# Kernel tuning notes

Measured on AMD Instinct MI355X. Metric: run time of the kernel, lower is better.

Reference implementation:

```python
import jax, jax.numpy as jnp
import numpy as np

# Hyperparameters from init_kwargs
SMOOTHNESS = 0.5
RADIUS_RATIO = 0.1  # computed in original code but never used in the mask math
IMG_SIZE = 512
BATCH = 32


def _smooth_mask(h, w, smoothness):
    """Vectorized replacement of the original per-pixel double loop.

    mask[i,j] = smoothness                       if |i-ch|^2 + |j-cw|^2 <= 1
              = max(1, dist_norm / smoothness)   otherwise
    where dist_norm = sqrt((|i-ch|/(h/2))^2 + (|j-cw|/(w/2))^2).
    Returns [h, w] float32 (broadcasts over the channel dim).
    """
    dh = jnp.abs(jnp.arange(h, dtype=jnp.float32) - (h // 2))[:, None]  # [h,1]
    dw = jnp.abs(jnp.arange(w, dtype=jnp.float32) - (w // 2))[None, :]  # [1,w]
    center = dh * dh + dw * dw <= 1.0
    dist = jnp.sqrt((dh / (h / 2)) ** 2 + (dw / (w / 2)) ** 2)
    outer = jnp.maximum(jnp.float32(1.0), dist / smoothness)
    return jnp.where(center, jnp.float32(smoothness), outer)


def setup_inputs() -> dict:
    key = jax.random.key(0)
    kx, = jax.random.split(key, 1)
    x = jax.random.normal(kx, (BATCH, 3, IMG_SIZE, IMG_SIZE), dtype=jnp.float32)
    param = jnp.ones((3, IMG_SIZE, IMG_SIZE), dtype=jnp.float32)  # nn.Parameter init
    return {"x": x, "param": param}


def reference(x, param):
    # x: [B, C, H, W] real -> complex spectrum, centered
    f = jnp.fft.fftshift(jnp.fft.fft2(x), axes=(-2, -1))
    h, w = x.shape[-2], x.shape[-1]
    mask = _smooth_mask(h, w, SMOOTHNESS)          # [H, W]
    filt = f * mask * param                        # broadcast [3,H,W] over batch
    out = jnp.fft.ifft2(jnp.fft.ifftshift(filt, axes=(-2, -1))).real
    return out
```

## Files before the change

### kernel.cpp

```cpp
#include <hip/hip_runtime.h>
#include <math.h>

#define N 512
#define CS 514
#define S8 0.70710678118654752440f

__device__ __forceinline__ float2 cadd(float2 a, float2 b){ return make_float2(a.x+b.x, a.y+b.y); }
__device__ __forceinline__ float2 csub(float2 a, float2 b){ return make_float2(a.x-b.x, a.y-b.y); }
__device__ __forceinline__ float2 cmul(float2 a, float2 b){
    return make_float2(fmaf(a.x,b.x,-(a.y*b.y)), fmaf(a.x,b.y, a.y*b.x));
}
template<int INV> __device__ __forceinline__ float2 rot90(float2 a){
    return INV ? make_float2(-a.y, a.x) : make_float2(a.y, -a.x);
}
template<int INV> __device__ __forceinline__ float2 rotW1(float2 a){
    return INV ? make_float2(S8*(a.x-a.y), S8*(a.x+a.y))
               : make_float2(S8*(a.x+a.y), S8*(a.y-a.x));
}
template<int INV> __device__ __forceinline__ float2 rotW3(float2 a){
    return INV ? make_float2(-S8*(a.x+a.y), S8*(a.x-a.y))
               : make_float2(S8*(a.y-a.x), -S8*(a.x+a.y));
}

template<int INV>
__device__ __forceinline__ void fft8(float2 v[8]) {
    float2 t0 = cadd(v[0],v[4]), t4 = csub(v[0],v[4]);
    float2 t1 = cadd(v[1],v[5]), t5 = rotW1<INV>(csub(v[1],v[5]));
    float2 t2 = cadd(v[2],v[6]), t6 = rot90<INV>(csub(v[2],v[6]));
    float2 t3 = cadd(v[3],v[7]), t7 = rotW3<INV>(csub(v[3],v[7]));
    float2 u0 = cadd(t0,t2), u2 = csub(t0,t2);
    float2 u1 = cadd(t1,t3), u3 = rot90<INV>(csub(t1,t3));
    float2 u4 = cadd(t4,t6), u6 = csub(t4,t6);
    float2 u5 = cadd(t5,t7), u7 = rot90<INV>(csub(t5,t7));
    v[0]=cadd(u0,u1); v[4]=csub(u0,u1);
    v[2]=cadd(u2,u3); v[6]=csub(u2,u3);
    v[1]=cadd(u4,u5); v[5]=csub(u4,u5);
    v[3]=cadd(u6,u7); v[7]=csub(u6,u7);
}

__device__ __forceinline__ void apply_pow(float2 v[8], float2 w1) {
    float2 w2 = cmul(w1,w1);
    float2 w3 = cmul(w2,w1);
    float2 w4 = cmul(w2,w2);
    v[1]=cmul(v[1],w1); v[2]=cmul(v[2],w2); v[3]=cmul(v[3],w3); v[4]=cmul(v[4],w4);
    v[5]=cmul(v[5],cmul(w4,w1));
    v[6]=cmul(v[6],cmul(w4,w2));
    v[7]=cmul(v[7],cmul(w4,w3));
}

__device__ __forceinline__ void fill_tw(float2* tw, int k) {
    float ang = -6.28318530717958647692f * (float)k / (float)N;
    float s, c; sincosf(ang, &s, &c);
    tw[k] = make_float2(c, s);
}

__device__ __forceinline__ void fft512_fwd(float2 v[8], int l, float2* sc, const float2* tw) {
    int hi = l >> 3, lo = l & 7;
    fft8<0>(v);
    apply_pow(v, tw[l]);
#pragma unroll
    for (int q = 0; q < 8; ++q) sc[q*64 + ((hi ^ q) << 3) + lo] = v[q];
#pragma unroll
    for (int b = 0; b < 8; ++b) v[b] = sc[hi*64 + ((b ^ hi) << 3) + lo];
    fft8<0>(v);
    apply_pow(v, tw[lo << 3]);
#pragma unroll
    for (int q2 = 0; q2 < 8; ++q2) sc[q2*64 + ((hi ^ q2) << 3) + (lo ^ hi)] = v[q2];
#pragma unroll
    for (int c = 0; c < 8; ++c) v[c] = sc[hi*64 + ((lo ^ hi) << 3) + (c ^ lo)];
    fft8<0>(v);
}

__device__ __forceinline__ void fft512_inv(float2 v[8], int l, float2* sc, const float2* tw) {
    int hi = l >> 3, lo = l & 7;
    fft8<1>(v);
#pragma unroll
    for (int c = 0; c < 8; ++c) sc[hi*64 + ((lo ^ hi) << 3) + (c ^ lo)] = v[c];
#pragma unroll
    for (int q2 = 0; q2 < 8; ++q2) v[q2] = sc[q2*64 + ((hi ^ q2) << 3) + (lo ^ hi)];
    {
        float2 w = tw[lo << 3];
        apply_pow(v, make_float2(w.x, -w.y));
    }
    fft8<1>(v);
#pragma unroll
    for (int b = 0; b < 8; ++b) sc[hi*64 + ((b ^ hi) << 3) + lo] = v[b];
#pragma unroll
    for (int q = 0; q < 8; ++q) v[q] = sc[q*64 + ((hi ^ q) << 3) + lo];
    {
        float2 w = tw[l];
        apply_pow(v, make_float2(w.x, -w.y));
    }
    fft8<1>(v);
}

__global__ __launch_bounds__(512) void k_filt(const float* __restrict__ param,
                                              float* __restrict__ filt) {
    int c = blockIdx.x >> 9;
    int vv = blockIdx.x & 511;
    int u = threadIdx.x;
    int dh = (u < 256) ? u : (512 - u);
    int dw = (vv < 256) ? vv : (512 - vv);
    int d2 = dh * dh + dw * dw;
    float m = (d2 <= 1) ? 0.5f : fmaxf(1.0f, sqrtf((float)d2) * (2.0f / 256.0f));
    int su  = (u + 256) & 511,  sv  = (vv + 256) & 511;
    int su2 = (256 - u) & 511,  sv2 = (256 - vv) & 511;
    float p  = param[((size_t)c * N + su)  * N + sv];
    float p2 = param[((size_t)c * N + su2) * N + sv2];
    const float invN2 = 1.0f / ((float)N * (float)N);
    filt[(((size_t)c << 9) + vv) * N + u] = m * 0.5f * (p + p2) * invN2;
}

__global__ __launch_bounds__(256) void k_row_fwd(const float* __restrict__ x,
                                                 float2* __restrict__ ws, int pairBase) {
    __shared__ float2 scr[4 * 512];
    __shared__ float2 tw[512];
    int t = threadIdx.x;
    int l = t & 63, wv = t >> 6;
    fill_tw(tw, t); fill_tw(tw, t + 256);
    __syncthreads();
    int pr = blockIdx.x >> 7;
    int row = ((blockIdx.x & 127) << 2) + wv;
    int pair = pairBase + pr;
    const float* xa = x + ((size_t)pair * N + row) * N;
    const float* xb = x + ((size_t)(pair + 48) * N + row) * N;
    float2 v[8];
#pragma unroll
    for (int a = 0; a < 8; ++a) v[a] = make_float2(xa[a * 64 + l], xb[a * 64 + l]);
    fft512_fwd(v, l, scr + wv * 512, tw);
    float2* o = ws + ((size_t)pr * N + row) * N;
#pragma unroll
    for (int r = 0; r < 8; ++r) o[r * 64 + l] = v[r];
}

__global__ __launch_bounds__(512) void k_col(float2* __restrict__ ws,
                                             const float* __restrict__ filt, int pairBase) {
    __shared__ float2 tile[8 * CS];
    __shared__ float2 tw[512];
    int t = threadIdx.x;
    int l = t & 63, wv = t >> 6;
    fill_tw(tw, t);
    int pr = blockIdx.x >> 6;
    int colBase = (blockIdx.x & 63) << 3;
    float2* wsImg = ws + (size_t)pr * (size_t)(N * N);

#pragma unroll
    for (int k = 0; k < 8; ++k) {
        int lin = (k << 9) + t;
        int r = lin >> 3, c = lin & 7;
        tile[c * CS + r] = wsImg[(size_t)r * N + colBase + c];
    }
    __syncthreads();

    float2* sc = tile + wv * CS;
    float2 v[8];
#pragma unroll
    for (int a = 0; a < 8; ++a) v[a] = sc[a * 64 + l];

    fft512_fwd(v, l, sc, tw);

    int ch = (pairBase + pr) % 3;
    int col = colBase + wv;
    const float* fcol = filt + (((size_t)ch << 9) + col) * N;
#pragma unroll
    for (int r = 0; r < 8; ++r) {
        float f = fcol[r * 64 + l];
        v[r].x *= f; v[r].y *= f;
    }

    fft512_inv(v, l, sc, tw);

#pragma unroll
    for (int a = 0; a < 8; ++a) sc[a * 64 + l] = v[a];
    __syncthreads();

#pragma unroll
    for (int k = 0; k < 8; ++k) {
        int lin = (k << 9) + t;
        int r = lin >> 3, c = lin & 7;
        wsImg[(size_t)r * N + colBase + c] = tile[c * CS + r];
    }
}

__global__ __launch_bounds__(256) void k_row_inv(const float2* __restrict__ ws,
                                                 float* __restrict__ out, int pairBase) {
    __shared__ float2 scr[4 * 512];
    __shared__ float2 tw[512];
    int t = threadIdx.x;
    int l = t & 63, wv = t >> 6;
    fill_tw(tw, t); fill_tw(tw, t + 256);
    __syncthreads();
    int pr = blockIdx.x >> 7;
    int row = ((blockIdx.x & 127) << 2) + wv;
    int pair = pairBase + pr;
    const float2* i0 = ws + ((size_t)pr * N + row) * N;
    float2 v[8];
#pragma unroll
    for (int r = 0; r < 8; ++r) v[r] = i0[r * 64 + l];
    fft512_inv(v, l, scr + wv * 512, tw);
    float* oa = out + ((size_t)pair * N + row) * N;
    float* ob = out + ((size_t)(pair + 48) * N + row) * N;
#pragma unroll
    for (int a = 0; a < 8; ++a) { oa[a * 64 + l] = v[a].x; ob[a * 64 + l] = v[a].y; }
}

extern "C" void kernel_launch(void* const* d_in, const int* in_sizes, int n_in,
                              void* d_out, int out_size, void* d_ws, size_t ws_size,
                              hipStream_t stream) {
    const float* x = (const float*)d_in[0];
    const float* param = (const float*)d_in[1];
    float* out = (float*)d_out;

    float* filt = (float*)d_ws;
    const size_t filtElems = (size_t)3 * N * N;
    float2* ws = (float2*)((char*)d_ws + filtElems * sizeof(float));

    const int NP = 48;
    size_t perImg = (size_t)N * N * sizeof(float2);
    size_t avail = (ws_size > filtElems * sizeof(float)) ? ws_size - filtElems * sizeof(float) : 0;
    int G = (int)(avail / perImg);
    if (G < 1) G = 1;
    if (G > NP) G = NP;

    k_filt<<<dim3(3 * N), dim3(N), 0, stream>>>(param, filt);

    for (int base = 0; base < NP; base += G) {
        int g = NP - base;
        if (g > G) g = G;
        k_row_fwd<<<dim3(g * 128), dim3(256), 0, stream>>>(x, ws, base);
        k_col<<<dim3(g * 64), dim3(512), 0, stream>>>(ws, filt, base);
        k_row_inv<<<dim3(g * 128), dim3(256), 0, stream>>>(ws, out, base);
    }
}
```

Baseline: 276.0 us.

## Vectorize global accesses to float4 and compute twiddles inline instead of via LDS tables

```diff
diff --git a/kernel.cpp b/kernel.cpp
--- a/kernel.cpp
+++ b/kernel.cpp
@@ -48,51 +48,46 @@
     v[7]=cmul(v[7],cmul(w4,w3));
 }
 
-__device__ __forceinline__ void fill_tw(float2* tw, int k) {
-    float ang = -6.28318530717958647692f * (float)k / (float)N;
-    float s, c; sincosf(ang, &s, &c);
-    tw[k] = make_float2(c, s);
-}
-
-__device__ __forceinline__ void fft512_fwd(float2 v[8], int l, float2* sc, const float2* tw) {
+#define TWO_PI 6.28318530717958647692f
+
+__device__ __forceinline__ void fft512_fwd(float2 v[8], int l, float2* sc) {
     int hi = l >> 3, lo = l & 7;
     fft8<0>(v);
-    apply_pow(v, tw[l]);
+    { float s, c; __sincosf(-TWO_PI * (1.0f/512.0f) * (float)l, &s, &c);
+      apply_pow(v, make_float2(c, s)); }
 #pragma unroll
     for (int q = 0; q < 8; ++q) sc[q*64 + ((hi ^ q) << 3) + lo] = v[q];
 #pragma unroll
     for (int b = 0; b < 8; ++b) v[b] = sc[hi*64 + ((b ^ hi) << 3) + lo];
     fft8<0>(v);
-    apply_pow(v, tw[lo << 3]);
+    { float s, c; __sincosf(-TWO_PI * (1.0f/64.0f) * (float)lo, &s, &c);
+      apply_pow(v, make_float2(c, s)); }
 #pragma unroll
     for (int q2 = 0; q2 < 8; ++q2) sc[q2*64 + ((hi ^ q2) << 3) + (lo ^ hi)] = v[q2];
 #pragma unroll
-    for (int c = 0; c < 8; ++c) v[c] = sc[hi*64 + ((lo ^ hi) << 3) + (c ^ lo)];
+    for (int cc = 0; cc < 8; ++cc) v[cc] = sc[hi*64 + ((lo ^ hi) << 3) + (cc ^ lo)];
     fft8<0>(v);
 }
 
-__device__ __forceinline__ void fft512_inv(float2 v[8], int l, float2* sc, const float2* tw) {
+__device__ __forceinline__ void fft512_inv(float2 v[8], int l, float2* sc) {
     int hi = l >> 3, lo = l & 7;
     fft8<1>(v);
 #pragma unroll
-    for (int c = 0; c < 8; ++c) sc[hi*64 + ((lo ^ hi) << 3) + (c ^ lo)] = v[c];
+    for (int cc = 0; cc < 8; ++cc) sc[hi*64 + ((lo ^ hi) << 3) + (cc ^ lo)] = v[cc];
 #pragma unroll
     for (int q2 = 0; q2 < 8; ++q2) v[q2] = sc[q2*64 + ((hi ^ q2) << 3) + (lo ^ hi)];
-    {
-        float2 w = tw[lo << 3];
-        apply_pow(v, make_float2(w.x, -w.y));
-    }
+    { float s, c; __sincosf(TWO_PI * (1.0f/64.0f) * (float)lo, &s, &c);
+      apply_pow(v, make_float2(c, s)); }
     fft8<1>(v);
 #pragma unroll
     for (int b = 0; b < 8; ++b) sc[hi*64 + ((b ^ hi) << 3) + lo] = v[b];
 #pragma unroll
     for (int q = 0; q < 8; ++q) v[q] = sc[q*64 + ((hi ^ q) << 3) + lo];
-    {
-        float2 w = tw[l];
-        apply_pow(v, make_float2(w.x, -w.y));
-    }
+    { float s, c; __sincosf(TWO_PI * (1.0f/512.0f) * (float)l, &s, &c);
+      apply_pow(v, make_float2(c, s)); }
     fft8<1>(v);
 }
+
 
 __global__ __launch_bounds__(512) void k_filt(const float* __restrict__ param,
                                               float* __restrict__ filt) {
@@ -108,47 +103,51 @@
     float p  = param[((size_t)c * N + su)  * N + sv];
     float p2 = param[((size_t)c * N + su2) * N + sv2];
     const float invN2 = 1.0f / ((float)N * (float)N);
-    filt[(((size_t)c << 9) + vv) * N + u] = m * 0.5f * (p + p2) * invN2;
+    int pos = ((vv >> 7) << 7) | ((vv & 63) << 1) | ((vv >> 6) & 1);
+    filt[(((size_t)c << 9) + pos) * N + u] = m * 0.5f * (p + p2) * invN2;
 }
 
 __global__ __launch_bounds__(256) void k_row_fwd(const float* __restrict__ x,
                                                  float2* __restrict__ ws, int pairBase) {
     __shared__ float2 scr[4 * 512];
-    __shared__ float2 tw[512];
     int t = threadIdx.x;
     int l = t & 63, wv = t >> 6;
-    fill_tw(tw, t); fill_tw(tw, t + 256);
-    __syncthreads();
     int pr = blockIdx.x >> 7;
     int row = ((blockIdx.x & 127) << 2) + wv;
     int pair = pairBase + pr;
-    const float* xa = x + ((size_t)pair * N + row) * N;
-    const float* xb = x + ((size_t)(pair + 48) * N + row) * N;
+    const float4* xa = (const float4*)(x + ((size_t)pair * N + row) * N);
+    const float4* xb = (const float4*)(x + ((size_t)(pair + 48) * N + row) * N);
+    float4 a0 = xa[l], a1 = xa[64 + l];
+    float4 b0 = xb[l], b1 = xb[64 + l];
+    float* s = (float*)(scr + wv * 512);
+    ((float4*)s)[l] = a0;       ((float4*)s)[64 + l]  = a1;
+    ((float4*)s)[128 + l] = b0; ((float4*)s)[192 + l] = b1;
     float2 v[8];
 #pragma unroll
-    for (int a = 0; a < 8; ++a) v[a] = make_float2(xa[a * 64 + l], xb[a * 64 + l]);
-    fft512_fwd(v, l, scr + wv * 512, tw);
-    float2* o = ws + ((size_t)pr * N + row) * N;
-#pragma unroll
-    for (int r = 0; r < 8; ++r) o[r * 64 + l] = v[r];
+    for (int a = 0; a < 8; ++a) v[a] = make_float2(s[a * 64 + l], s[512 + a * 64 + l]);
+    fft512_fwd(v, l, scr + wv * 512);
+    float4* o = (float4*)(ws + ((size_t)pr * N + row) * N);
+#pragma unroll
+    for (int j = 0; j < 4; ++j)
+        o[j * 64 + l] = make_float4(v[2*j].x, v[2*j].y, v[2*j+1].x, v[2*j+1].y);
 }
 
 __global__ __launch_bounds__(512) void k_col(float2* __restrict__ ws,
                                              const float* __restrict__ filt, int pairBase) {
     __shared__ float2 tile[8 * CS];
-    __shared__ float2 tw[512];
     int t = threadIdx.x;
     int l = t & 63, wv = t >> 6;
-    fill_tw(tw, t);
     int pr = blockIdx.x >> 6;
     int colBase = (blockIdx.x & 63) << 3;
     float2* wsImg = ws + (size_t)pr * (size_t)(N * N);
 
 #pragma unroll
-    for (int k = 0; k < 8; ++k) {
-        int lin = (k << 9) + t;
+    for (int k = 0; k < 4; ++k) {
+        int lin = (k << 10) + (t << 1);
         int r = lin >> 3, c = lin & 7;
-        tile[c * CS + r] = wsImg[(size_t)r * N + colBase + c];
+        float4 f = *(const float4*)(&wsImg[(size_t)r * N + colBase + c]);
+        tile[c * CS + r]       = make_float2(f.x, f.y);
+        tile[(c + 1) * CS + r] = make_float2(f.z, f.w);
     }
     __syncthreads();
 
@@ -157,7 +156,7 @@
 #pragma unroll
     for (int a = 0; a < 8; ++a) v[a] = sc[a * 64 + l];
 
-    fft512_fwd(v, l, sc, tw);
+    fft512_fwd(v, l, sc);
 
     int ch = (pairBase + pr) % 3;
     int col = colBase + wv;
@@ -168,40 +167,47 @@
         v[r].x *= f; v[r].y *= f;
     }
 
-    fft512_inv(v, l, sc, tw);
+    fft512_inv(v, l, sc);
 
 #pragma unroll
     for (int a = 0; a < 8; ++a) sc[a * 64 + l] = v[a];
     __syncthreads();
 
 #pragma unroll
-    for (int k = 0; k < 8; ++k) {
-        int lin = (k << 9) + t;
+    for (int k = 0; k < 4; ++k) {
+        int lin = (k << 10) + (t << 1);
         int r = lin >> 3, c = lin & 7;
-        wsImg[(size_t)r * N + colBase + c] = tile[c * CS + r];
+        float2 e0 = tile[c * CS + r], e1 = tile[(c + 1) * CS + r];
+        *(float4*)(&wsImg[(size_t)r * N + colBase + c]) = make_float4(e0.x, e0.y, e1.x, e1.y);
     }
 }
 
 __global__ __launch_bounds__(256) void k_row_inv(const float2* __restrict__ ws,
                                                  float* __restrict__ out, int pairBase) {
     __shared__ float2 scr[4 * 512];
-    __shared__ float2 tw[512];
     int t = threadIdx.x;
     int l = t & 63, wv = t >> 6;
-    fill_tw(tw, t); fill_tw(tw, t + 256);
-    __syncthreads();
     int pr = blockIdx.x >> 7;
     int row = ((blockIdx.x & 127) << 2) + wv;
     int pair = pairBase + pr;
-    const float2* i0 = ws + ((size_t)pr * N + row) * N;
+    const float4* i4 = (const float4*)(ws + ((size_t)pr * N + row) * N);
     float2 v[8];
 #pragma unroll
-    for (int r = 0; r < 8; ++r) v[r] = i0[r * 64 + l];
-    fft512_inv(v, l, scr + wv * 512, tw);
-    float* oa = out + ((size_t)pair * N + row) * N;
-    float* ob = out + ((size_t)(pair + 48) * N + row) * N;
-#pragma unroll
-    for (int a = 0; a < 8; ++a) { oa[a * 64 + l] = v[a].x; ob[a * 64 + l] = v[a].y; }
+    for (int j = 0; j < 4; ++j) {
+        float4 f = i4[j * 64 + l];
+        v[2*j]   = make_float2(f.x, f.y);
+        v[2*j+1] = make_float2(f.z, f.w);
+    }
+    fft512_inv(v, l, scr + wv * 512);
+    float* s = (float*)(scr + wv * 512);
+#pragma unroll
+    for (int a = 0; a < 8; ++a) { s[a*64 + l] = v[a].x; s[512 + a*64 + l] = v[a].y; }
+    float4* oa = (float4*)(out + ((size_t)pair * N + row) * N);
+    float4* ob = (float4*)(out + ((size_t)(pair + 48) * N + row) * N);
+    oa[l]      = ((float4*)s)[l];
+    oa[64 + l] = ((float4*)s)[64 + l];
+    ob[l]      = ((float4*)s)[128 + l];
+    ob[64 + l] = ((float4*)s)[192 + l];
 }
 
 extern "C" void kernel_launch(void* const* d_in, const int* in_sizes, int n_in,
```

After: 271.6 us. No clear change (-1.6%).
